# Kernel optimization log

Hardware: AMD Instinct MI355X
Metric: run time of the kernel (lower is better)

## Reference

```python
import jax, jax.numpy as jnp
import numpy as np

B, T, C = 4, 2048, 1024
H = 16
D = C // H  # 64


def setup_inputs() -> dict:
    key = jax.random.key(0)
    k1, k2, k3 = jax.random.split(key, 3)
    x = jax.random.normal(k1, (B, T, C), dtype=jnp.float32)
    W_attn = jax.random.normal(k2, (C, 3 * C), dtype=jnp.float32) * (1.0 / np.sqrt(C))
    W_proj = jax.random.normal(k3, (C, C), dtype=jnp.float32) * (1.0 / np.sqrt(C))
    return {"x": x, "W_attn": W_attn, "W_proj": W_proj}


def reference(x, W_attn, W_proj):
    b, t, c = x.shape
    # qkv projection: [B,T,3C]
    qkv = jnp.einsum('btc,cd->btd', x, W_attn)
    q, k, v = jnp.split(qkv, 3, axis=-1)
    # split heads -> [B,H,T,D]
    q = q.reshape(b, t, H, D).transpose(0, 2, 1, 3)
    k = k.reshape(b, t, H, D).transpose(0, 2, 1, 3)
    v = v.reshape(b, t, H, D).transpose(0, 2, 1, 3)
    # scores scaled by 1/sqrt(C) (faithful to source: uses full embed dim)
    att = jnp.einsum('bhtd,bhsd->bhts', q, k) * (1.0 / jnp.sqrt(jnp.float32(c)))
    # causal mask: -inf where key index > query index
    causal = jnp.tril(jnp.ones((t, t), dtype=bool))
    att = jnp.where(causal, att, jnp.float32(-jnp.inf))
    att = jax.nn.softmax(att, axis=-1)
    # attention output -> combine heads
    y = jnp.einsum('bhts,bhsd->bhtd', att, v)
    y = y.transpose(0, 2, 1, 3).reshape(b, t, c)
    z = jnp.einsum('btc,cd->btd', y, W_proj)
    return z
```

## Files before the change

### kernel.cpp

```cpp
#include <hip/hip_runtime.h>
#include <hip/hip_bf16.h>

typedef __bf16 bf16x8 __attribute__((ext_vector_type(8)));
typedef float f32x4 __attribute__((ext_vector_type(4)));

static __device__ __forceinline__ __bf16 tobf(float x) {
    __hip_bfloat16 h = __float2bfloat16(x);
    __bf16 r;
    __builtin_memcpy(&r, &h, 2);
    return r;
}

static __device__ __forceinline__ float fexp2(float x) {
    float r;
    asm("v_exp_f32 %0, %1" : "=v"(r) : "v"(x));
    return r;
}

__global__ __launch_bounds__(256) void prep_k(const float* __restrict__ x,
                                              __hip_bfloat16* __restrict__ x_bf,
                                              const float* __restrict__ Wa,
                                              __hip_bfloat16* __restrict__ WaT,
                                              const float* __restrict__ Wp,
                                              __hip_bfloat16* __restrict__ WpT) {
    __shared__ float tile[32][33];
    const int bid = blockIdx.x;
    const int tid = threadIdx.x;
    if (bid < 8192) {
        int i = bid * 256 + tid;
        float4 v = reinterpret_cast<const float4*>(x)[i];
        __hip_bfloat16 a = __float2bfloat16(v.x);
        __hip_bfloat16 b = __float2bfloat16(v.y);
        __hip_bfloat16 c = __float2bfloat16(v.z);
        __hip_bfloat16 d = __float2bfloat16(v.w);
        ushort4 o;
        o.x = *reinterpret_cast<unsigned short*>(&a);
        o.y = *reinterpret_cast<unsigned short*>(&b);
        o.z = *reinterpret_cast<unsigned short*>(&c);
        o.w = *reinterpret_cast<unsigned short*>(&d);
        reinterpret_cast<ushort4*>(x_bf)[i] = o;
        return;
    }
    const float* in;
    __hip_bfloat16* out;
    int bx, Cn, qrows;
    float qscale;
    int t;
    if (bid < 8192 + 3072) {
        t = bid - 8192;
        in = Wa; out = WaT; Cn = 3072; qrows = 1024;
        qscale = 0.045084223f;
        bx = t % 96;
    } else {
        t = bid - 11264;
        in = Wp; out = WpT; Cn = 1024; qrows = 0;
        qscale = 1.0f;
        bx = t % 32;
    }
    const int by = (bid < 11264) ? (t / 96) : (t / 32);
    const int R = 1024;
    const int c0 = bx * 32, r0 = by * 32;
    const int tx = tid & 31, ty = tid >> 5;
#pragma unroll
    for (int i = 0; i < 4; ++i)
        tile[ty + i * 8][tx] = in[(size_t)(r0 + ty + i * 8) * Cn + c0 + tx];
    __syncthreads();
#pragma unroll
    for (int i = 0; i < 4; ++i) {
        int orow = c0 + ty + i * 8;
        float v = tile[tx][ty + i * 8];
        if (orow < qrows) v *= qscale;
        out[(size_t)orow * R + r0 + tx] = __float2bfloat16(v);
    }
}

__global__ __launch_bounds__(256) void vtrans_k(const __hip_bfloat16* __restrict__ qkv,
                                                __hip_bfloat16* __restrict__ Vt) {
    __shared__ __attribute__((aligned(16))) __hip_bfloat16 lds[64 * 72];
    const int tt = blockIdx.x;
    const int bh = blockIdx.y;
    const int b = bh >> 4, h = bh & 15;
    const int tid = threadIdx.x;
    const __hip_bfloat16* src =
        qkv + (size_t)b * 2048 * 3072 + 2048 + h * 64 + (size_t)tt * 64 * 3072;
#pragma unroll
    for (int p = 0; p < 2; ++p) {
        int u = p * 256 + tid;
        int t_in = u >> 3, dc = u & 7;
        bf16x8 v = *reinterpret_cast<const bf16x8*>(src + (size_t)t_in * 3072 + dc * 8);
        *reinterpret_cast<bf16x8*>(&lds[t_in * 72 + dc * 8]) = v;
    }
    __syncthreads();
    __hip_bfloat16* dst = Vt + (size_t)bh * 64 * 2048 + tt * 64;
#pragma unroll
    for (int p = 0; p < 2; ++p) {
        int w = p * 256 + tid;
        int d = w >> 3, oc = w & 7;
        bf16x8 o;
#pragma unroll
        for (int e = 0; e < 8; ++e) {
            int s = oc * 8 + e;
            int r = (s & 3) | (((s >> 3) & 3) << 2) | (((s >> 2) & 1) << 4);
            int t_in = (s & 32) | r;
            o[e] = lds[t_in * 72 + d];
        }
        *reinterpret_cast<bf16x8*>(&dst[(size_t)d * 2048 + oc * 8]) = o;
    }
}

template <bool OUT_BF16>
__global__ __launch_bounds__(256) void gemm_bt(const __hip_bfloat16* __restrict__ A,
                                               const __hip_bfloat16* __restrict__ Bt,
                                               __hip_bfloat16* __restrict__ Cb,
                                               float* __restrict__ Cf,
                                               int M, int N, int K) {
    __shared__ __attribute__((aligned(16))) char As[128 * 128];
    __shared__ __attribute__((aligned(16))) char Bs[128 * 128];
    const int tid = threadIdx.x;
    const int lane = tid & 63, wid = tid >> 6;
    const int l15 = lane & 15, lg = lane >> 4;
    const int wr = wid >> 1, wc = wid & 1;
    const int lin = blockIdx.y * gridDim.x + blockIdx.x;
    const int cpx = (gridDim.x * gridDim.y) >> 3;
    const int sw = (lin & 7) * cpx + (lin >> 3);
    const int bn = sw % gridDim.x, bm = sw / gridDim.x;
    const size_t arow0 = (size_t)bm * 128;
    const size_t brow0 = (size_t)bn * 128;

    f32x4 acc[4][4] = {};

    const int nk = K >> 6;
    for (int kt = 0; kt < nk; ++kt) {
        __syncthreads();
        {
            const int k0 = kt * 64;
#pragma unroll
            for (int p = 0; p < 4; ++p) {
                int idx = p * 256 + tid;
                int row = idx >> 3;
                int c = idx & 7;
                int col = 8 * (c ^ (row & 7));
                const __hip_bfloat16* ga = A + (arow0 + row) * (size_t)K + k0 + col;
                const __hip_bfloat16* gb = Bt + (brow0 + row) * (size_t)K + k0 + col;
                __builtin_amdgcn_global_load_lds(
                    (const __attribute__((address_space(1))) void*)ga,
                    (__attribute__((address_space(3))) void*)(&As[idx * 16]), 16, 0, 0);
                __builtin_amdgcn_global_load_lds(
                    (const __attribute__((address_space(1))) void*)gb,
                    (__attribute__((address_space(3))) void*)(&Bs[idx * 16]), 16, 0, 0);
            }
        }
        __syncthreads();
        const int swz = l15 & 7;
#pragma unroll
        for (int ks = 0; ks < 2; ++ks) {
            bf16x8 af[4], bfr[4];
#pragma unroll
            for (int m = 0; m < 4; ++m)
                af[m] = *reinterpret_cast<const bf16x8*>(
                    &As[(wr * 64 + m * 16 + l15) * 128 + 16 * ((ks * 4 + lg) ^ swz)]);
#pragma unroll
            for (int n = 0; n < 4; ++n)
                bfr[n] = *reinterpret_cast<const bf16x8*>(
                    &Bs[(wc * 64 + n * 16 + l15) * 128 + 16 * ((ks * 4 + lg) ^ swz)]);
#pragma unroll
            for (int m = 0; m < 4; ++m)
#pragma unroll
                for (int n = 0; n < 4; ++n)
                    acc[m][n] = __builtin_amdgcn_mfma_f32_16x16x32_bf16(af[m], bfr[n], acc[m][n], 0, 0, 0);
        }
    }

#pragma unroll
    for (int m = 0; m < 4; ++m) {
#pragma unroll
        for (int n = 0; n < 4; ++n) {
#pragma unroll
            for (int j = 0; j < 4; ++j) {
                int row = bm * 128 + wr * 64 + m * 16 + lg * 4 + j;
                int col = bn * 128 + wc * 64 + n * 16 + l15;
                if (OUT_BF16)
                    Cb[(size_t)row * N + col] = __float2bfloat16(acc[m][n][j]);
                else
                    Cf[(size_t)row * N + col] = acc[m][n][j];
            }
        }
    }
}

__global__ __launch_bounds__(256) void attn_k(const __hip_bfloat16* __restrict__ qkv,
                                              const __hip_bfloat16* __restrict__ Vt,
                                              __hip_bfloat16* __restrict__ y) {
    constexpr int TT = 2048;
    constexpr int S3C = 3072;
    const int bh = blockIdx.x, b = bh >> 4, h = bh & 15;
    const int tid = threadIdx.x;
    const int wid = tid >> 6, lane = tid & 63;
    const int l15 = lane & 15, lg = lane >> 4;

    __shared__ __attribute__((aligned(16))) char Ks[3][64 * 128];
    __shared__ __attribute__((aligned(16))) char Vs[3][64 * 128];

    const __hip_bfloat16* base = qkv + (size_t)b * TT * S3C;
    const int qo = h * 64, ko = 1024 + h * 64;
    const __hip_bfloat16* vt = Vt + (size_t)bh * 64 * TT;

    bf16x8 vones;
#pragma unroll
    for (int i = 0; i < 8; ++i) vones[i] = tobf(1.0f);

    const int idx0 = tid, idx1 = 256 + tid;
    const int r0 = idx0 >> 3, c0 = 8 * ((idx0 & 7) ^ (r0 & 7));
    const int r1 = idx1 >> 3, c1 = 8 * ((idx1 & 7) ^ (r1 & 7));

#pragma unroll 1
    for (int pass = 0; pass < 2; ++pass) {
        const int st = pass == 0 ? (15 - (int)blockIdx.y) : (int)blockIdx.y;
        const int qbase = st * 128 + wid * 32;
        const int my_nt = (qbase >> 6) + 1;
        const int blk_nt = st * 2 + 2;

        bf16x8 aq[2][2];
#pragma unroll
        for (int m = 0; m < 2; ++m) {
            const __hip_bfloat16* qp = base + (size_t)(qbase + m * 16 + l15) * S3C + qo + lg * 8;
            aq[m][0] = *reinterpret_cast<const bf16x8*>(qp);
            aq[m][1] = *reinterpret_cast<const bf16x8*>(qp + 32);
        }

        f32x4 acc[2][4] = {};
        f32x4 lsum[2] = {};

        const __hip_bfloat16* kp0 = base + (size_t)r0 * S3C + ko + c0;
        const __hip_bfloat16* kp1 = base + (size_t)r1 * S3C + ko + c1;
        const __hip_bfloat16* vp0 = vt + (size_t)r0 * TT + c0;
        const __hip_bfloat16* vp1 = vt + (size_t)r1 * TT + c1;

        auto stage = [&](int buf) {
            char* Kd = &Ks[buf][0];
            char* Vd = &Vs[buf][0];
            __builtin_amdgcn_global_load_lds(
                (const __attribute__((address_space(1))) void*)kp0,
                (__attribute__((address_space(3))) void*)(Kd + idx0 * 16), 16, 0, 0);
            __builtin_amdgcn_global_load_lds(
                (const __attribute__((address_space(1))) void*)kp1,
                (__attribute__((address_space(3))) void*)(Kd + idx1 * 16), 16, 0, 0);
            __builtin_amdgcn_global_load_lds(
                (const __attribute__((address_space(1))) void*)vp0,
                (__attribute__((address_space(3))) void*)(Vd + idx0 * 16), 16, 0, 0);
            __builtin_amdgcn_global_load_lds(
                (const __attribute__((address_space(1))) void*)vp1,
                (__attribute__((address_space(3))) void*)(Vd + idx1 * 16), 16, 0, 0);
            kp0 += (size_t)64 * S3C;
            kp1 += (size_t)64 * S3C;
            vp0 += 64;
            vp1 += 64;
        };

        stage(0);
        stage(1);
        asm volatile("s_waitcnt vmcnt(4)" ::: "memory");
        __syncthreads();

        int bc = 0;
        for (int kt = 0; kt < blk_nt; ++kt) {
            const bool more = (kt + 2 < blk_nt);
            if (more) {
                int bs = bc + 2;
                if (bs >= 3) bs -= 3;
                stage(bs);
            }
            if (kt < my_nt) {
                const int kb = kt * 64;
                const char* Kb = &Ks[bc][0];
                const char* Vb = &Vs[bc][0];
                const int swl = l15 & 7;
                f32x4 s[2][4];
                __builtin_amdgcn_s_setprio(1);
#pragma unroll
                for (int cg = 0; cg < 4; ++cg) {
                    const char* krow = Kb + (cg * 16 + l15) * 128;
                    bf16x8 k0 = *reinterpret_cast<const bf16x8*>(krow + 16 * (lg ^ swl));
                    bf16x8 k1 = *reinterpret_cast<const bf16x8*>(krow + 16 * ((4 + lg) ^ swl));
#pragma unroll
                    for (int m = 0; m < 2; ++m) {
                        f32x4 z = {0.f, 0.f, 0.f, 0.f};
                        z = __builtin_amdgcn_mfma_f32_16x16x32_bf16(k0, aq[m][0], z, 0, 0, 0);
                        z = __builtin_amdgcn_mfma_f32_16x16x32_bf16(k1, aq[m][1], z, 0, 0, 0);
                        s[m][cg] = z;
                    }
                }
                __builtin_amdgcn_s_setprio(0);
                bf16x8 vb[2][4];
#pragma unroll
                for (int dg = 0; dg < 4; ++dg) {
                    const char* vrow = Vb + (dg * 16 + l15) * 128;
                    vb[0][dg] = *reinterpret_cast<const bf16x8*>(vrow + 16 * (lg ^ swl));
                    vb[1][dg] = *reinterpret_cast<const bf16x8*>(vrow + 16 * ((4 + lg) ^ swl));
                }
                float p[2][4][4];
                const bool needmask = (kb + 63 > qbase);
#pragma unroll
                for (int m = 0; m < 2; ++m)
#pragma unroll
                    for (int cg = 0; cg < 4; ++cg)
#pragma unroll
                        for (int j = 0; j < 4; ++j) {
                            float e = fexp2(s[m][cg][j]);
                            if (needmask) {
                                int key = kb + cg * 16 + lg * 4 + j;
                                int qrow = qbase + m * 16 + l15;
                                e = (key > qrow) ? 0.f : e;
                            }
                            p[m][cg][j] = e;
                        }
                bf16x8 pa[2][2];
#pragma unroll
                for (int m = 0; m < 2; ++m)
#pragma unroll
                    for (int ks = 0; ks < 2; ++ks) {
                        bf16x8 tt2;
                        tt2[0] = tobf(p[m][2 * ks][0]);
                        tt2[1] = tobf(p[m][2 * ks][1]);
                        tt2[2] = tobf(p[m][2 * ks][2]);
                        tt2[3] = tobf(p[m][2 * ks][3]);
                        tt2[4] = tobf(p[m][2 * ks + 1][0]);
                        tt2[5] = tobf(p[m][2 * ks + 1][1]);
                        tt2[6] = tobf(p[m][2 * ks + 1][2]);
                        tt2[7] = tobf(p[m][2 * ks + 1][3]);
                        pa[m][ks] = tt2;
                    }
                __builtin_amdgcn_s_setprio(1);
#pragma unroll
                for (int ks = 0; ks < 2; ++ks) {
#pragma unroll
                    for (int dg = 0; dg < 4; ++dg)
#pragma unroll
                        for (int m = 0; m < 2; ++m)
                            acc[m][dg] = __builtin_amdgcn_mfma_f32_16x16x32_bf16(
                                pa[m][ks], vb[ks][dg], acc[m][dg], 0, 0, 0);
#pragma unroll
                    for (int m = 0; m < 2; ++m)
                        lsum[m] = __builtin_amdgcn_mfma_f32_16x16x32_bf16(pa[m][ks], vones,
                                                                          lsum[m], 0, 0, 0);
                }
                __builtin_amdgcn_s_setprio(0);
            }
            if (more)
                asm volatile("s_waitcnt vmcnt(4)" ::: "memory");
            else
                asm volatile("s_waitcnt vmcnt(0)" ::: "memory");
            __syncthreads();
            bc = (bc == 2) ? 0 : bc + 1;
        }

#pragma unroll
        for (int m = 0; m < 2; ++m)
#pragma unroll
            for (int j = 0; j < 4; ++j) {
                float inv = 1.f / lsum[m][j];
                int t = qbase + m * 16 + lg * 4 + j;
#pragma unroll
                for (int dg = 0; dg < 4; ++dg) {
                    float o = acc[m][dg][j] * inv;
                    y[((size_t)(b * TT + t)) * 1024 + h * 64 + dg * 16 + l15] = __float2bfloat16(o);
                }
            }
        __syncthreads();
    }
}

extern "C" void kernel_launch(void* const* d_in, const int* in_sizes, int n_in,
                              void* d_out, int out_size, void* d_ws, size_t ws_size,
                              hipStream_t stream) {
    const float* x = (const float*)d_in[0];
    const float* Wa = (const float*)d_in[1];
    const float* Wp = (const float*)d_in[2];
    float* out = (float*)d_out;

    __hip_bfloat16* ws = (__hip_bfloat16*)d_ws;
    __hip_bfloat16* x_bf = ws;
    __hip_bfloat16* WaT = x_bf + (size_t)8192 * 1024;
    __hip_bfloat16* WpT = WaT + (size_t)3072 * 1024;
    __hip_bfloat16* qkv = WpT + (size_t)1024 * 1024;
    __hip_bfloat16* ybf = qkv + (size_t)8192 * 3072;
    __hip_bfloat16* Vt = ybf + (size_t)8192 * 1024;

    prep_k<<<8192 + 3072 + 1024, 256, 0, stream>>>(x, x_bf, Wa, WaT, Wp, WpT);
    gemm_bt<true><<<dim3(24, 64), 256, 0, stream>>>(x_bf, WaT, qkv, nullptr, 8192, 3072, 1024);
    vtrans_k<<<dim3(32, 64), 256, 0, stream>>>(qkv, Vt);
    attn_k<<<dim3(64, 8), 256, 0, stream>>>(qkv, Vt, ybf);
    gemm_bt<false><<<dim3(8, 64), 256, 0, stream>>>(ybf, WpT, nullptr, out, 8192, 1024, 1024);
}
```

Before: 173.3 us.

## Rewrite GEMM as 8-wave 128x256 double-buffered kernel; attention to double buffering

Replaces the 4-wave 128x128 GEMM with a 512-thread kernel computing 128x256 tiles with K-step 32. It double-buffers LDS so the next tile's global-to-LDS loads overlap the current MFMAs, and uses a new paired-row swizzled layout. Attention drops from triple to double buffering with a full vmcnt(0) wait per iteration, and the trailing barrier is removed. This trades prefetch depth for lower LDS use and larger GEMM tiles for fewer blocks, so grids get smaller.

New measurement: 171.3 us. About the same (-1.2%).

```diff
diff --git a/kernel.cpp b/kernel.cpp
--- a/kernel.cpp
+++ b/kernel.cpp
@@ -109,80 +109,103 @@
 }
 
 template <bool OUT_BF16>
-__global__ __launch_bounds__(256) void gemm_bt(const __hip_bfloat16* __restrict__ A,
-                                               const __hip_bfloat16* __restrict__ Bt,
-                                               __hip_bfloat16* __restrict__ Cb,
-                                               float* __restrict__ Cf,
-                                               int M, int N, int K) {
-    __shared__ __attribute__((aligned(16))) char As[128 * 128];
-    __shared__ __attribute__((aligned(16))) char Bs[128 * 128];
+__global__ __launch_bounds__(512, 4) void gemm8w(const __hip_bfloat16* __restrict__ A,
+                                                 const __hip_bfloat16* __restrict__ Bt,
+                                                 __hip_bfloat16* __restrict__ Cb,
+                                                 float* __restrict__ Cf,
+                                                 int M, int N, int K) {
+    __shared__ __attribute__((aligned(16))) char As[2][64 * 128];
+    __shared__ __attribute__((aligned(16))) char Bs[2][128 * 128];
     const int tid = threadIdx.x;
     const int lane = tid & 63, wid = tid >> 6;
     const int l15 = lane & 15, lg = lane >> 4;
-    const int wr = wid >> 1, wc = wid & 1;
+    const int wr = wid >> 2, wc = wid & 3;
     const int lin = blockIdx.y * gridDim.x + blockIdx.x;
     const int cpx = (gridDim.x * gridDim.y) >> 3;
     const int sw = (lin & 7) * cpx + (lin >> 3);
     const int bn = sw % gridDim.x, bm = sw / gridDim.x;
     const size_t arow0 = (size_t)bm * 128;
-    const size_t brow0 = (size_t)bn * 128;
+    const size_t brow0 = (size_t)bn * 256;
 
     f32x4 acc[4][4] = {};
 
-    const int nk = K >> 6;
+    const int arp = tid >> 3, apu = (tid & 7) ^ (arp & 7);
+    const int aR = 2 * arp + (apu >> 2), aC = (apu & 3) * 8;
+    const int b1i = 512 + tid;
+    const int brp1 = b1i >> 3, bpu1 = (b1i & 7) ^ (brp1 & 7);
+    const int bR1 = 2 * brp1 + (bpu1 >> 2), bC1 = (bpu1 & 3) * 8;
+
+    const __hip_bfloat16* pa = A + (arow0 + aR) * (size_t)K + aC;
+    const __hip_bfloat16* pb0 = Bt + (brow0 + aR) * (size_t)K + aC;
+    const __hip_bfloat16* pb1 = Bt + (brow0 + bR1) * (size_t)K + bC1;
+
+    auto stage = [&](int buf) {
+        char* Ad = &As[buf][0];
+        char* Bd = &Bs[buf][0];
+        __builtin_amdgcn_global_load_lds(
+            (const __attribute__((address_space(1))) void*)pa,
+            (__attribute__((address_space(3))) void*)(Ad + tid * 16), 16, 0, 0);
+        __builtin_amdgcn_global_load_lds(
+            (const __attribute__((address_space(1))) void*)pb0,
+            (__attribute__((address_space(3))) void*)(Bd + tid * 16), 16, 0, 0);
+        __builtin_amdgcn_global_load_lds(
+            (const __attribute__((address_space(1))) void*)pb1,
+            (__attribute__((address_space(3))) void*)(Bd + (512 + tid) * 16), 16, 0, 0);
+        pa += 32;
+        pb0 += 32;
+        pb1 += 32;
+    };
+
+    stage(0);
+    asm volatile("s_waitcnt vmcnt(0)" ::: "memory");
+    __syncthreads();
+
+    const int nk = K >> 5;
+    int cur = 0;
     for (int kt = 0; kt < nk; ++kt) {
+        if (kt + 1 < nk) stage(cur ^ 1);
+        const char* Ab = cur ? &As[1][0] : &As[0][0];
+        const char* Bb = cur ? &Bs[1][0] : &Bs[0][0];
+        bf16x8 af[4], bfr[4];
+#pragma unroll
+        for (int mf = 0; mf < 4; ++mf) {
+            int R = wr * 64 + mf * 16 + l15;
+            int rp = R >> 1;
+            int p = (((R & 1) << 2) + lg) ^ (rp & 7);
+            af[mf] = *reinterpret_cast<const bf16x8*>(Ab + rp * 128 + p * 16);
+        }
+#pragma unroll
+        for (int nf = 0; nf < 4; ++nf) {
+            int R = wc * 64 + nf * 16 + l15;
+            int rp = R >> 1;
+            int p = (((R & 1) << 2) + lg) ^ (rp & 7);
+            bfr[nf] = *reinterpret_cast<const bf16x8*>(Bb + rp * 128 + p * 16);
+        }
+        __builtin_amdgcn_s_setprio(1);
+#pragma unroll
+        for (int mf = 0; mf < 4; ++mf)
+#pragma unroll
+            for (int nf = 0; nf < 4; ++nf)
+                acc[mf][nf] = __builtin_amdgcn_mfma_f32_16x16x32_bf16(af[mf], bfr[nf],
+                                                                      acc[mf][nf], 0, 0, 0);
+        __builtin_amdgcn_s_setprio(0);
+        asm volatile("s_waitcnt vmcnt(0)" ::: "memory");
         __syncthreads();
-        {
-            const int k0 = kt * 64;
-#pragma unroll
-            for (int p = 0; p < 4; ++p) {
-                int idx = p * 256 + tid;
-                int row = idx >> 3;
-                int c = idx & 7;
-                int col = 8 * (c ^ (row & 7));
-                const __hip_bfloat16* ga = A + (arow0 + row) * (size_t)K + k0 + col;
-                const __hip_bfloat16* gb = Bt + (brow0 + row) * (size_t)K + k0 + col;
-                __builtin_amdgcn_global_load_lds(
-                    (const __attribute__((address_space(1))) void*)ga,
-                    (__attribute__((address_space(3))) void*)(&As[idx * 16]), 16, 0, 0);
-                __builtin_amdgcn_global_load_lds(
-                    (const __attribute__((address_space(1))) void*)gb,
-                    (__attribute__((address_space(3))) void*)(&Bs[idx * 16]), 16, 0, 0);
-            }
-        }
-        __syncthreads();
-        const int swz = l15 & 7;
-#pragma unroll
-        for (int ks = 0; ks < 2; ++ks) {
-            bf16x8 af[4], bfr[4];
-#pragma unroll
-            for (int m = 0; m < 4; ++m)
-                af[m] = *reinterpret_cast<const bf16x8*>(
-                    &As[(wr * 64 + m * 16 + l15) * 128 + 16 * ((ks * 4 + lg) ^ swz)]);
-#pragma unroll
-            for (int n = 0; n < 4; ++n)
-                bfr[n] = *reinterpret_cast<const bf16x8*>(
-                    &Bs[(wc * 64 + n * 16 + l15) * 128 + 16 * ((ks * 4 + lg) ^ swz)]);
-#pragma unroll
-            for (int m = 0; m < 4; ++m)
-#pragma unroll
-                for (int n = 0; n < 4; ++n)
-                    acc[m][n] = __builtin_amdgcn_mfma_f32_16x16x32_bf16(af[m], bfr[n], acc[m][n], 0, 0, 0);
-        }
-    }
-
-#pragma unroll
-    for (int m = 0; m < 4; ++m) {
-#pragma unroll
-        for (int n = 0; n < 4; ++n) {
+        cur ^= 1;
+    }
+
+#pragma unroll
+    for (int mf = 0; mf < 4; ++mf) {
+#pragma unroll
+        for (int nf = 0; nf < 4; ++nf) {
 #pragma unroll
             for (int j = 0; j < 4; ++j) {
-                int row = bm * 128 + wr * 64 + m * 16 + lg * 4 + j;
-                int col = bn * 128 + wc * 64 + n * 16 + l15;
+                int row = bm * 128 + wr * 64 + mf * 16 + lg * 4 + j;
+                int col = bn * 256 + wc * 64 + nf * 16 + l15;
                 if (OUT_BF16)
-                    Cb[(size_t)row * N + col] = __float2bfloat16(acc[m][n][j]);
+                    Cb[(size_t)row * N + col] = __float2bfloat16(acc[mf][nf][j]);
                 else
-                    Cf[(size_t)row * N + col] = acc[m][n][j];
+                    Cf[(size_t)row * N + col] = acc[mf][nf][j];
             }
         }
     }
@@ -198,8 +221,8 @@
     const int wid = tid >> 6, lane = tid & 63;
     const int l15 = lane & 15, lg = lane >> 4;
 
-    __shared__ __attribute__((aligned(16))) char Ks[3][64 * 128];
-    __shared__ __attribute__((aligned(16))) char Vs[3][64 * 128];
+    __shared__ __attribute__((aligned(16))) char Ks[2][64 * 128];
+    __shared__ __attribute__((aligned(16))) char Vs[2][64 * 128];
 
     const __hip_bfloat16* base = qkv + (size_t)b * TT * S3C;
     const int qo = h * 64, ko = 1024 + h * 64;
@@ -237,8 +260,8 @@
         const __hip_bfloat16* vp1 = vt + (size_t)r1 * TT + c1;
 
         auto stage = [&](int buf) {
-            char* Kd = &Ks[buf][0];
-            char* Vd = &Vs[buf][0];
+            char* Kd = buf ? &Ks[1][0] : &Ks[0][0];
+            char* Vd = buf ? &Vs[1][0] : &Vs[0][0];
             __builtin_amdgcn_global_load_lds(
                 (const __attribute__((address_space(1))) void*)kp0,
                 (__attribute__((address_space(3))) void*)(Kd + idx0 * 16), 16, 0, 0);
@@ -258,22 +281,16 @@
         };
 
         stage(0);
-        stage(1);
-        asm volatile("s_waitcnt vmcnt(4)" ::: "memory");
+        asm volatile("s_waitcnt vmcnt(0)" ::: "memory");
         __syncthreads();
 
-        int bc = 0;
+        int cur = 0;
         for (int kt = 0; kt < blk_nt; ++kt) {
-            const bool more = (kt + 2 < blk_nt);
-            if (more) {
-                int bs = bc + 2;
-                if (bs >= 3) bs -= 3;
-                stage(bs);
-            }
+            if (kt + 1 < blk_nt) stage(cur ^ 1);
             if (kt < my_nt) {
                 const int kb = kt * 64;
-                const char* Kb = &Ks[bc][0];
-                const char* Vb = &Vs[bc][0];
+                const char* Kb = cur ? &Ks[1][0] : &Ks[0][0];
+                const char* Vb = cur ? &Vs[1][0] : &Vs[0][0];
                 const int swl = l15 & 7;
                 f32x4 s[2][4];
                 __builtin_amdgcn_s_setprio(1);
@@ -346,12 +363,9 @@
                 }
                 __builtin_amdgcn_s_setprio(0);
             }
-            if (more)
-                asm volatile("s_waitcnt vmcnt(4)" ::: "memory");
-            else
-                asm volatile("s_waitcnt vmcnt(0)" ::: "memory");
+            asm volatile("s_waitcnt vmcnt(0)" ::: "memory");
             __syncthreads();
-            bc = (bc == 2) ? 0 : bc + 1;
+            cur ^= 1;
         }
 
 #pragma unroll
@@ -366,7 +380,6 @@
                     y[((size_t)(b * TT + t)) * 1024 + h * 64 + dg * 16 + l15] = __float2bfloat16(o);
                 }
             }
-        __syncthreads();
     }
 }
 
@@ -387,8 +400,8 @@
     __hip_bfloat16* Vt = ybf + (size_t)8192 * 1024;
 
     prep_k<<<8192 + 3072 + 1024, 256, 0, stream>>>(x, x_bf, Wa, WaT, Wp, WpT);
-    gemm_bt<true><<<dim3(24, 64), 256, 0, stream>>>(x_bf, WaT, qkv, nullptr, 8192, 3072, 1024);
+    gemm8w<true><<<dim3(12, 64), 512, 0, stream>>>(x_bf, WaT, qkv, nullptr, 8192, 3072, 1024);
     vtrans_k<<<dim3(32, 64), 256, 0, stream>>>(qkv, Vt);
     attn_k<<<dim3(64, 8), 256, 0, stream>>>(qkv, Vt, ybf);
-    gemm_bt<false><<<dim3(8, 64), 256, 0, stream>>>(ybf, WpT, nullptr, out, 8192, 1024, 1024);
-}
+    gemm8w<false><<<dim3(4, 64), 512, 0, stream>>>(ybf, WpT, nullptr, out, 8192, 1024, 1024);
+}
```
